# Kernel tuning notes

Hardware: AMD Instinct MI355X
Metric: run time of the kernel (lower is better)

## Reference

```python
import jax, jax.numpy as jnp
import numpy as np

NBATCH, NUP, NDOWN, NMO, NCONF = 8192, 8, 8, 32, 64


def setup_inputs() -> dict:
    key = jax.random.key(0)
    k1, k2, k3, k4 = jax.random.split(key, 4)
    MO = jax.random.normal(k1, (NBATCH, NUP + NDOWN, NMO), dtype=jnp.float32)
    d2MO = jax.random.normal(k2, (NBATCH, NUP + NDOWN, NMO), dtype=jnp.float32)
    # each config = 8 distinct MO column indices per spin (distinct -> invertible A)
    configs_up = jnp.argsort(jax.random.uniform(k3, (NCONF, NMO)), axis=1)[:, :NUP].astype(jnp.int32)
    configs_down = jnp.argsort(jax.random.uniform(k4, (NCONF, NMO)), axis=1)[:, :NDOWN].astype(jnp.int32)
    return {"MO": MO, "d2MO": d2MO, "configs_up": configs_up, "configs_down": configs_down}


def _gather(M, elec_idx, cols):
    # M: (B, nelec, nmo) -> select electron rows then per-config MO columns
    Ms = M[:, elec_idx, :]                  # (B, n, nmo)
    A = jnp.take(Ms, cols, axis=2)          # (B, n, C, n)
    return jnp.transpose(A, (0, 2, 1, 3))   # (B, C, n, n)


def reference(MO, d2MO, configs_up, configs_down):
    nup = configs_up.shape[1]
    ndown = configs_down.shape[1]
    iup = jnp.arange(nup)
    idown = jnp.arange(nup, nup + ndown)

    Aup = _gather(MO, iup, configs_up)       # (B, C, nup, nup)
    Adn = _gather(MO, idown, configs_down)   # (B, C, ndown, ndown)
    d2up = _gather(d2MO, iup, configs_up)
    d2dn = _gather(d2MO, idown, configs_down)

    iAup = jnp.linalg.inv(Aup)
    iAdn = jnp.linalg.inv(Adn)

    # btrace(iA @ d2A) = sum_ij iA[i,j] * d2A[j,i]
    tr = lambda X, Y: jnp.einsum('bcij,bcji->bc', X, Y)
    out = tr(iAup, d2up) + tr(iAdn, d2dn)    # (B, C)

    # return_local_energy=False branch: multiply by product of determinants
    pd = jnp.linalg.det(Aup) * jnp.linalg.det(Adn)
    return -0.5 * out * pd
```

## Files before the change

kernel.cpp:

```cpp
#include <hip/hip_runtime.h>

#define NBATCH 8192
#define NELEC  16
#define NMO    32
#define NCONF  64
#define NS     8
#define TSTR   20
#define TSZ    (NMO * TSTR)
#define TSTRH  24
#define TSZH   (NMO * TSTRH)

typedef float    v2f   __attribute__((ext_vector_type(2)));
typedef _Float16 half8 __attribute__((ext_vector_type(8)));

__device__ __forceinline__ v2f pkfma(v2f a, v2f b, v2f c) {
#if __has_builtin(__builtin_elementwise_fma)
    return __builtin_elementwise_fma(a, b, c);
#else
    return a * b + c;
#endif
}
__device__ __forceinline__ v2f bc2(float s) { return (v2f){s, s}; }
__device__ __forceinline__ float getel2(const v2f (&R)[4], int j) {
    return (j & 1) ? R[j >> 1].y : R[j >> 1].x;
}
__device__ __forceinline__ void setel2(v2f (&R)[4], int j, float v) {
    if (j & 1) R[j >> 1].y = v; else R[j >> 1].x = v;
}

__device__ __forceinline__ void solve8T(const float* __restrict__ MOT,
                                        const _Float16* __restrict__ D2T,
                                        const int (&cols)[NS], int eoff,
                                        float& det_out, float& tr_out)
{
    v2f A2[NS][4];
    #pragma unroll
    for (int j = 0; j < NS; ++j) {
        const float4* pa = (const float4*)(MOT + cols[j] * TSTR + eoff);
        float4 a0 = pa[0], a1 = pa[1];
        A2[j][0] = (v2f){a0.x, a0.y};
        A2[j][1] = (v2f){a0.z, a0.w};
        A2[j][2] = (v2f){a1.x, a1.y};
        A2[j][3] = (v2f){a1.z, a1.w};
    }

    float det = 1.0f;
    #pragma unroll
    for (int k = 0; k < NS; ++k) {
        float ukk = getel2(A2[k], k);
        det *= ukk;
        float pinv = __builtin_amdgcn_rcpf(ukk);
        #pragma unroll
        for (int r = k + 1; r < NS; ++r) {
            float m = getel2(A2[r], k) * pinv;
            v2f m2 = bc2(m);
            #pragma unroll
            for (int p = (k + 1) >> 1; p < 4; ++p)
                A2[r][p] = pkfma(-m2, A2[k][p], A2[r][p]);
            setel2(A2[r], k, m);
        }
        setel2(A2[k], k, pinv);
    }

    float tr = 0.0f;
    #pragma unroll
    for (int t = 0; t < 4; ++t) {
        const int k0 = 2 * t, k1 = 2 * t + 1;

        half8 hd0 = *(const half8*)(D2T + cols[k0] * TSTRH + eoff);
        half8 hd1 = *(const half8*)(D2T + cols[k1] * TSTRH + eoff);

        v2f y2[NS];
        y2[k0] = (v2f){1.0f, 0.0f};
        y2[k1] = (v2f){-getel2(A2[k1], k0), 1.0f};
        #pragma unroll
        for (int i = k1 + 1; i < NS; ++i) {
            v2f acc = (v2f){0.0f, 0.0f};
            #pragma unroll
            for (int j = k0; j < i; ++j)
                acc = pkfma(bc2(getel2(A2[i], j)), y2[j], acc);
            y2[i] = -acc;
        }

        v2f x2[NS];
        #pragma unroll
        for (int i = NS - 1; i >= 0; --i) {
            v2f acc = (i >= k0) ? y2[i] : (v2f){0.0f, 0.0f};
            #pragma unroll
            for (int c2 = i + 1; c2 < NS; ++c2)
                acc = pkfma(-bc2(getel2(A2[i], c2)), x2[c2], acc);
            x2[i] = acc * bc2(getel2(A2[i], i));
        }

        #pragma unroll
        for (int i = 0; i < NS; ++i) {
            tr = fmaf(x2[i].x, (float)hd0[i], tr);
            tr = fmaf(x2[i].y, (float)hd1[i], tr);
        }
    }

    det_out = det;
    tr_out  = tr;
}

__global__ __launch_bounds__(256)
void kp_dh_kernel(const float* __restrict__ MO,
                  const float* __restrict__ d2MO,
                  const int*   __restrict__ cfg_up,
                  const int*   __restrict__ cfg_dn,
                  float*       __restrict__ out)
{
    __shared__ float    smemA[2][TSZ];
    __shared__ _Float16 smemD[2][TSZH];

    const int tid  = threadIdx.x;
    const int half = tid >> 7;
    const int u    = tid & 127;
    const int b    = blockIdx.x * 2 + half;

    float*    MOT = smemA[half];
    _Float16* D2T = smemD[half];

    const float* MOb = MO   + (size_t)b * NELEC * NMO;
    const float* d2b = d2MO + (size_t)b * NELEC * NMO;

    {
        int r = u >> 3;
        int c = (u & 7) * 4;
        float4 v = *(const float4*)(MOb + r * NMO + c);
        float4 w = *(const float4*)(d2b + r * NMO + c);
        MOT[(c + 0) * TSTR + r] = v.x;
        MOT[(c + 1) * TSTR + r] = v.y;
        MOT[(c + 2) * TSTR + r] = v.z;
        MOT[(c + 3) * TSTR + r] = v.w;
        D2T[(c + 0) * TSTRH + r] = (_Float16)w.x;
        D2T[(c + 1) * TSTRH + r] = (_Float16)w.y;
        D2T[(c + 2) * TSTRH + r] = (_Float16)w.z;
        D2T[(c + 3) * TSTRH + r] = (_Float16)w.w;
    }
    __syncthreads();

    const int cidx = u >> 1;
    const int s    = u & 1;
    const int* cfg = s ? cfg_dn : cfg_up;
    int4 c0 = ((const int4*)cfg)[cidx * 2 + 0];
    int4 c1 = ((const int4*)cfg)[cidx * 2 + 1];
    const int cols[NS] = {c0.x, c0.y, c0.z, c0.w, c1.x, c1.y, c1.z, c1.w};

    float det, tr;
    solve8T(MOT, D2T, cols, s * NS, det, tr);

    float det_o = __shfl_xor(det, 1);
    float tr_o  = __shfl_xor(tr, 1);
    if (s == 0)
        out[(size_t)b * NCONF + cidx] = -0.5f * (tr + tr_o) * det * det_o;
}

extern "C" void kernel_launch(void* const* d_in, const int* in_sizes, int n_in,
                              void* d_out, int out_size, void* d_ws, size_t ws_size,
                              hipStream_t stream)
{
    const float* MO     = (const float*)d_in[0];
    const float* d2MO   = (const float*)d_in[1];
    const int*   cfg_up = (const int*)d_in[2];
    const int*   cfg_dn = (const int*)d_in[3];
    float* out = (float*)d_out;

    dim3 grid(NBATCH / 2);
    dim3 block(256);
    kp_dh_kernel<<<grid, block, 0, stream>>>(MO, d2MO, cfg_up, cfg_dn, out);
}
```

Baseline: 89.01 us.

## Sort config columns per wavefront, vectorize transpose stores, exchange spin results via LDS

Each thread's 8 column indices are sorted with a sorting network, and the permutation parity is tracked to fix the determinant sign. This makes LDS gather addresses more ordered across lanes, which may reduce bank conflicts. Threads are remapped so each 64-lane wavefront holds a single spin, which removes divergence in config loads, and the up/down results are combined through shared memory plus an extra barrier instead of a lane shuffle. The transpose into LDS now uses coalesced scalar global loads and vectorized float4/half4 LDS stores. The cost is extra compare-swap ALU work and a second __syncthreads.

```diff
diff --git a/kernel.cpp b/kernel.cpp
--- a/kernel.cpp
+++ b/kernel.cpp
@@ -12,6 +12,7 @@
 
 typedef float    v2f   __attribute__((ext_vector_type(2)));
 typedef _Float16 half8 __attribute__((ext_vector_type(8)));
+typedef _Float16 half4 __attribute__((ext_vector_type(4)));
 
 __device__ __forceinline__ v2f pkfma(v2f a, v2f b, v2f c) {
 #if __has_builtin(__builtin_elementwise_fma)
@@ -112,6 +113,8 @@
 {
     __shared__ float    smemA[2][TSZ];
     __shared__ _Float16 smemD[2][TSZH];
+    __shared__ float    xtr [2][NCONF];
+    __shared__ float    xdet[2][NCONF];
 
     const int tid  = threadIdx.x;
     const int half = tid >> 7;
@@ -125,35 +128,45 @@
     const float* d2b = d2MO + (size_t)b * NELEC * NMO;
 
     {
-        int r = u >> 3;
-        int c = (u & 7) * 4;
-        float4 v = *(const float4*)(MOb + r * NMO + c);
-        float4 w = *(const float4*)(d2b + r * NMO + c);
-        MOT[(c + 0) * TSTR + r] = v.x;
-        MOT[(c + 1) * TSTR + r] = v.y;
-        MOT[(c + 2) * TSTR + r] = v.z;
-        MOT[(c + 3) * TSTR + r] = v.w;
-        D2T[(c + 0) * TSTRH + r] = (_Float16)w.x;
-        D2T[(c + 1) * TSTRH + r] = (_Float16)w.y;
-        D2T[(c + 2) * TSTRH + r] = (_Float16)w.z;
-        D2T[(c + 3) * TSTRH + r] = (_Float16)w.w;
+        const int c  = u & 31;
+        const int r0 = (u >> 5) << 2;
+        const float* pa = MOb + r0 * NMO + c;
+        const float* pd = d2b + r0 * NMO + c;
+        float a0 = pa[0 * NMO], a1 = pa[1 * NMO], a2 = pa[2 * NMO], a3 = pa[3 * NMO];
+        float d0 = pd[0 * NMO], d1 = pd[1 * NMO], d2 = pd[2 * NMO], d3 = pd[3 * NMO];
+        *(float4*)(MOT + c * TSTR + r0) = make_float4(a0, a1, a2, a3);
+        *(half4*)(D2T + c * TSTRH + r0) =
+            (half4){(_Float16)d0, (_Float16)d1, (_Float16)d2, (_Float16)d3};
     }
+
+    const int s    = (tid >> 6) & 1;
+    const int cidx = tid & 63;
+    const int* cfg = s ? cfg_dn : cfg_up;
+    int4 q0 = ((const int4*)cfg)[cidx * 2 + 0];
+    int4 q1 = ((const int4*)cfg)[cidx * 2 + 1];
+    int cols[NS] = {q0.x, q0.y, q0.z, q0.w, q1.x, q1.y, q1.z, q1.w};
+    int sgn = 0;
+    #define CE(i, j) { int ai = cols[i], aj = cols[j]; int sw = ai > aj; \
+                       cols[i] = sw ? aj : ai; cols[j] = sw ? ai : aj; sgn ^= sw; }
+    CE(0,1) CE(2,3) CE(0,2) CE(1,3) CE(1,2)
+    CE(4,5) CE(6,7) CE(4,6) CE(5,7) CE(5,6)
+    CE(0,4) CE(2,6) CE(2,4)
+    CE(1,5) CE(3,7) CE(3,5)
+    CE(1,2) CE(3,4) CE(5,6)
+    #undef CE
+    const float fsign = sgn ? -1.0f : 1.0f;
+
     __syncthreads();
-
-    const int cidx = u >> 1;
-    const int s    = u & 1;
-    const int* cfg = s ? cfg_dn : cfg_up;
-    int4 c0 = ((const int4*)cfg)[cidx * 2 + 0];
-    int4 c1 = ((const int4*)cfg)[cidx * 2 + 1];
-    const int cols[NS] = {c0.x, c0.y, c0.z, c0.w, c1.x, c1.y, c1.z, c1.w};
 
     float det, tr;
     solve8T(MOT, D2T, cols, s * NS, det, tr);
+    det *= fsign;
 
-    float det_o = __shfl_xor(det, 1);
-    float tr_o  = __shfl_xor(tr, 1);
-    if (s == 0)
-        out[(size_t)b * NCONF + cidx] = -0.5f * (tr + tr_o) * det * det_o;
+    if (s) { xtr[half][cidx] = tr; xdet[half][cidx] = det; }
+    __syncthreads();
+    if (!s)
+        out[(size_t)b * NCONF + cidx] =
+            -0.5f * (tr + xtr[half][cidx]) * det * xdet[half][cidx];
 }
 
 extern "C" void kernel_launch(void* const* d_in, const int* in_sizes, int n_in,
```

After: 89.68 us. About the same (+0.7%).
